# Performance work log

Hardware: AMD Instinct MI355X
Metric: run time of the kernel (lower is better)

The kernel has to match this reference:

```python
import jax, jax.numpy as jnp
import numpy as np

HEADS = 6
POINTS = 4
INJ_SHAPES = ((96, 96), (48, 48), (24, 24))  # adapter pyramid (H_l, W_l), sum = 12096 tokens
EXT_SHAPES = ((48, 48),)                      # vit grid level


def layernorm(x, g, b, eps=1e-6):
    m = jnp.mean(x, axis=-1, keepdims=True)
    v = jnp.mean((x - m) ** 2, axis=-1, keepdims=True)
    return (x - m) * jax.lax.rsqrt(v + eps) * g + b


def bilinear_sample(img, loc):
    # img: [B, heads, H, W, D]; loc: [B, heads, P, 2] normalized (x, y) in [0, 1]
    # matches F.grid_sample(mode='bilinear', padding_mode='zeros', align_corners=False)
    B, nh, H, W, D = img.shape
    flat = img.reshape(B, nh, H * W, D)
    ix = loc[..., 0] * W - 0.5
    iy = loc[..., 1] * H - 0.5
    x0f = jnp.floor(ix)
    y0f = jnp.floor(iy)
    wx = (ix - x0f)[..., None]
    wy = (iy - y0f)[..., None]
    x0 = x0f.astype(jnp.int32)
    y0 = y0f.astype(jnp.int32)

    def gather(xi, yi):
        valid = (xi >= 0) & (xi < W) & (yi >= 0) & (yi < H)
        idx = jnp.clip(yi, 0, H - 1) * W + jnp.clip(xi, 0, W - 1)
        g = jnp.take_along_axis(flat, idx[..., None], axis=2)
        return g * valid[..., None]

    v00 = gather(x0, y0)
    v01 = gather(x0 + 1, y0)
    v10 = gather(x0, y0 + 1)
    v11 = gather(x0 + 1, y0 + 1)
    return (v00 * (1 - wx) + v01 * wx) * (1 - wy) + (v10 * (1 - wx) + v11 * wx) * wy


def msda(query, value, ref, shapes, Wv, bv, Ws, bs_, Wa, ba, Wo, bo):
    # mmcv MultiScaleDeformableAttention (batch_first) without dropout/identity.
    B, Lq, C = query.shape
    D = C // HEADS
    L = len(shapes)
    v = (value @ Wv + bv).reshape(B, -1, HEADS, D)
    off = (query @ Ws + bs_).reshape(B, Lq, HEADS, L, POINTS, 2)
    aw = jax.nn.softmax((query @ Wa + ba).reshape(B, Lq, HEADS, L * POINTS), axis=-1)
    aw = aw.reshape(B, Lq, HEADS, L, POINTS)
    norm = jnp.array([[w, h] for (h, w) in shapes], dtype=query.dtype)  # (x, y) normalizer
    # ref: [B, Lq, 1, 2] broadcasts over heads/levels/points
    loc = ref[:, :, None, :, None, :] + off / norm[None, None, None, :, None, :]
    starts = np.cumsum([0] + [h * w for h, w in shapes])
    out = jnp.zeros((B, HEADS, Lq, D), query.dtype)
    for l, (h, w) in enumerate(shapes):
        vl = v[:, starts[l]:starts[l + 1]].reshape(B, h, w, HEADS, D).transpose(0, 3, 1, 2, 4)
        ll = loc[:, :, :, l].transpose(0, 2, 1, 3, 4).reshape(B, HEADS, Lq * POINTS, 2)
        s = bilinear_sample(vl, ll).reshape(B, HEADS, Lq, POINTS, D)
        out = out + jnp.einsum('bhqp,bhqpd->bhqd', aw[:, :, :, l].transpose(0, 2, 1, 3), s)
    out = out.transpose(0, 2, 1, 3).reshape(B, Lq, C)
    return out @ Wo + bo


def setup_inputs() -> dict:
    key = jax.random.key(0)
    ks = jax.random.split(key, 24)
    B, Hh, Ww, C = 1, 48, 48, 768
    NA = 12096  # 4*HW + HW + HW/4
    f32 = jnp.float32
    lin = lambda k, i, o, s=0.02: jax.random.normal(k, (i, o), f32) * s
    p = {
        'vit_feats': jax.random.normal(ks[0], (B, Hh, Ww, C), f32),
        'adapter_feats': jax.random.normal(ks[1], (B, NA, C), f32),
        'ref1': jax.random.uniform(ks[2], (B, Hh * Ww, 1, 2), f32),
        'ref2': jax.random.uniform(ks[3], (B, NA, 1, 2), f32),
        'inj_qn_g': jnp.ones((C,), f32), 'inj_qn_b': jnp.zeros((C,), f32),
        'inj_Wv': lin(ks[4], C, C), 'inj_bv': jnp.zeros((C,), f32),
        'inj_Ws': lin(ks[5], C, HEADS * 3 * POINTS * 2, 0.01),
        'inj_bs': jax.random.normal(ks[6], (HEADS * 3 * POINTS * 2,), f32),
        'inj_Wa': lin(ks[7], C, HEADS * 3 * POINTS), 'inj_ba': jnp.zeros((HEADS * 3 * POINTS,), f32),
        'inj_Wo': lin(ks[8], C, C), 'inj_bo': jnp.zeros((C,), f32),
        'inj_gamma': jax.random.normal(ks[9], (C,), f32) * 0.1,
        'ext_vn_g': jnp.ones((C,), f32), 'ext_vn_b': jnp.zeros((C,), f32),
        'ext_qn_g': jnp.ones((C,), f32), 'ext_qn_b': jnp.zeros((C,), f32),
        'ext_Wv': lin(ks[10], C, C), 'ext_bv': jnp.zeros((C,), f32),
        'ext_Ws': lin(ks[11], C, HEADS * 1 * POINTS * 2, 0.01),
        'ext_bs': jax.random.normal(ks[12], (HEADS * 1 * POINTS * 2,), f32),
        'ext_Wa': lin(ks[13], C, HEADS * 1 * POINTS), 'ext_ba': jnp.zeros((HEADS * 1 * POINTS,), f32),
        'ext_Wo': lin(ks[14], C, C), 'ext_bo': jnp.zeros((C,), f32),
        'H': 48, 'W': 48,
    }
    return p


def reference(vit_feats, adapter_feats, ref1, ref2,
              inj_qn_g, inj_qn_b, inj_Wv, inj_bv, inj_Ws, inj_bs, inj_Wa, inj_ba, inj_Wo, inj_bo, inj_gamma,
              ext_vn_g, ext_vn_b, ext_qn_g, ext_qn_b, ext_Wv, ext_bv, ext_Ws, ext_bs, ext_Wa, ext_ba, ext_Wo, ext_bo,
              H, W):
    b, h, w, c = vit_feats.shape
    q = vit_feats.reshape(b, h * w, c)
    # Injector: query = vit tokens, value = 3-level adapter pyramid; identity = 0, gamma-scaled residual
    attn = msda(layernorm(q, inj_qn_g, inj_qn_b), adapter_feats, ref1, INJ_SHAPES,
                inj_Wv, inj_bv, inj_Ws, inj_bs, inj_Wa, inj_ba, inj_Wo, inj_bo)
    q = q + inj_gamma * attn
    vit_out = q.reshape(b, h, w, c)
    # Extractor (with_cffn=False, v_pre_norm=True): value = LN(vit tokens), identity = adapter query, post query-norm
    value = layernorm(q, ext_vn_g, ext_vn_b)
    attn2 = msda(adapter_feats, value, ref2, EXT_SHAPES,
                 ext_Wv, ext_bv, ext_Ws, ext_bs, ext_Wa, ext_ba, ext_Wo, ext_bo)
    adapter_out = layernorm(adapter_feats + attn2, ext_qn_g, ext_qn_b)
    return vit_out, adapter_out
```

## Files before the change

### kernel.cpp

```cpp
#include <hip/hip_runtime.h>


#define LQ_VIT 2304
#define NA_ADA 12096

typedef float f32x4 __attribute__((ext_vector_type(4)));
typedef short bf16x8 __attribute__((ext_vector_type(8)));

__device__ __forceinline__ unsigned short f2bf(float f) {
  unsigned u = __builtin_bit_cast(unsigned, f);
  u += 0x7FFFu + ((u >> 16) & 1u);
  return (unsigned short)(u >> 16);
}
__device__ __forceinline__ float bf2f(unsigned short u) {
  return __builtin_bit_cast(float, (unsigned)u << 16);
}
__device__ __forceinline__ f32x4 ld4bf(const unsigned short* p) {
  ushort4 t = *(const ushort4*)p;
  f32x4 r; r[0] = bf2f(t.x); r[1] = bf2f(t.y); r[2] = bf2f(t.z); r[3] = bf2f(t.w);
  return r;
}

__device__ __forceinline__ void gload_lds16(const void* g, void* l) {
  __builtin_amdgcn_global_load_lds(
      (__attribute__((address_space(1))) void*)(void*)g,
      (__attribute__((address_space(3))) void*)l, 16, 0, 0);
}

struct PrepPack {
  const float* W[8];
  unsigned short* WT[8];
  int N[8];
  int cum[9];
  const float* adapter; unsigned short* adbf; int n4;
  const float* vit; const float* qg; const float* qb; unsigned short* qln;
  const float* isv; const float* iav; const float* ibv;
  const float* esv; const float* eav;
  float* bci; float* bbig;
};

__global__ __launch_bounds__(256) void prep_kernel(PrepPack pp) {
  int b = blockIdx.x;
  int tid = threadIdx.x;
  if (b < 2568) {
    int kb = b / 107, col = b % 107;
    int z = 0;
#pragma unroll
    for (int i = 0; i < 8; i++) if (col >= pp.cum[i + 1]) z = i + 1;
    int nb = col - pp.cum[z];
    const float* __restrict__ W = pp.W[z];
    unsigned short* __restrict__ WT = pp.WT[z];
    int N = pp.N[z];
    int kb32 = kb * 32, nb32 = nb * 32;
    __shared__ float tile[32][33];
    int tx = tid & 31, ty = tid >> 5;
    for (int i = ty; i < 32; i += 8) {
      int n = nb32 + tx;
      tile[i][tx] = (n < N) ? W[(size_t)(kb32 + i) * N + n] : 0.f;
    }
    __syncthreads();
    for (int i = ty; i < 32; i += 8) {
      int n = nb32 + i, k = kb32 + tx;
      if (n < N) WT[(size_t)n * 768 + k] = f2bf(tile[tx][i]);
    }
  } else if (b < 4616) {
    for (int i = (b - 2568) * 256 + tid; i < pp.n4; i += 2048 * 256) {
      float4 v = ((const float4*)pp.adapter)[i];
      ushort4 o;
      o.x = f2bf(v.x); o.y = f2bf(v.y); o.z = f2bf(v.z); o.w = f2bf(v.w);
      ((ushort4*)pp.adbf)[i] = o;
    }
  } else if (b < 5192) {
    int wid = (b - 4616) * 4 + (tid >> 6);
    int lane = tid & 63;
    if (wid >= LQ_VIT) return;
    const float* row = pp.vit + (size_t)wid * 768;
    float x[12]; float s = 0.f;
#pragma unroll
    for (int j = 0; j < 12; j++) { x[j] = row[lane + j * 64]; s += x[j]; }
#pragma unroll
    for (int o = 32; o >= 1; o >>= 1) s += __shfl_xor(s, o);
    float mean = s * (1.f / 768.f);
    float v = 0.f;
#pragma unroll
    for (int j = 0; j < 12; j++) { float d = x[j] - mean; v += d * d; }
#pragma unroll
    for (int o = 32; o >= 1; o >>= 1) v += __shfl_xor(v, o);
    float rs = rsqrtf(v * (1.f / 768.f) + 1e-6f);
#pragma unroll
    for (int j = 0; j < 12; j++) {
      int c = lane + j * 64;
      pp.qln[(size_t)wid * 768 + c] = f2bf((x[j] - mean) * rs * pp.qg[c] + pp.qb[c]);
    }
  } else {
    for (int i = tid; i < 840; i += 256) {
      if (i < 144) pp.bci[i] = pp.isv[i];
      else if (i < 216) pp.bci[i] = pp.iav[i - 144];
      if (i < 768) pp.bbig[i] = pp.ibv[i];
      else if (i < 816) pp.bbig[i] = pp.esv[i - 768];
      else pp.bbig[i] = pp.eav[i - 816];
    }
  }
}

struct GemmTask {
  const unsigned short* A; const unsigned short* BT;
  const float* bias; unsigned short* C;
  int M, N, NT, nwg;
};

__global__ __launch_bounds__(256, 2) void gemm_big_kernel(GemmTask t0, GemmTask t1, int split) {
  __shared__ unsigned short lds[2][(128 + 128) * 64];

  GemmTask tk = (blockIdx.x < split) ? t0 : t1;
  int id = (blockIdx.x < split) ? blockIdx.x : blockIdx.x - split;
  int nwg = tk.nwg;
  int qq = nwg >> 3, rr = nwg & 7;
  int xcd = id & 7, idx = id >> 3;
  int wg = (xcd < rr ? xcd * (qq + 1) : rr * (qq + 1) + (xcd - rr) * qq) + idx;
  int nt = wg % tk.NT, mt = wg / tk.NT;
  int m0 = mt * 128, n0 = nt * 128;
  int M = tk.M, N = tk.N;
  const unsigned short* __restrict__ A = tk.A;
  const unsigned short* __restrict__ BT = tk.BT;
  const int K = 768, kT = 12;

  int tid = threadIdx.x;
  int w = tid >> 6, lane = tid & 63;
  int wr = w >> 1, wc = w & 1;
  int frow = lane & 15, ghi = lane >> 4;
  int l7 = lane & 7;
  int sr = lane >> 3;
  int sgx = ((l7 ^ sr) * 8);
  int gx0 = ((ghi ^ l7) * 8);
  int gx1 = (((4 + ghi) ^ l7) * 8);

  f32x4 acc[4][4] = {};

  auto stage = [&](unsigned short* dst, int k0) {
#pragma unroll
    for (int i = 0; i < 8; i++) {
      int c = w * 8 + i;
      if (c < 16) {
        int gm = m0 + c * 8 + sr; if (gm >= M) gm = M - 1;
        gload_lds16(&A[(size_t)gm * K + k0 + sgx], &dst[c * 512]);
      } else {
        int gn = n0 + (c - 16) * 8 + sr; if (gn >= N) gn = N - 1;
        gload_lds16(&BT[(size_t)gn * K + k0 + sgx], &dst[c * 512]);
      }
    }
  };

  unsigned short* b0 = &lds[0][0];
  unsigned short* b1 = &lds[1][0];
  stage(b0, 0);
  __syncthreads();

  for (int t = 0; t < kT; t++) {
    unsigned short* cb = (t & 1) ? b1 : b0;
    unsigned short* nb = (t & 1) ? b0 : b1;
    if (t + 1 < kT) stage(nb, (t + 1) << 6);
    const unsigned short* As_ = cb;
    const unsigned short* Bs_ = cb + 16 * 512;
    bf16x8 af0[4], af1[4], bg0[4], bg1[4];
#pragma unroll
    for (int m = 0; m < 4; m++) {
      int r = wr * 64 + m * 16 + frow;
      af0[m] = *(const bf16x8*)&As_[r * 64 + gx0];
      af1[m] = *(const bf16x8*)&As_[r * 64 + gx1];
    }
#pragma unroll
    for (int n = 0; n < 4; n++) {
      int r = wc * 64 + n * 16 + frow;
      bg0[n] = *(const bf16x8*)&Bs_[r * 64 + gx0];
      bg1[n] = *(const bf16x8*)&Bs_[r * 64 + gx1];
    }
#pragma unroll
    for (int m = 0; m < 4; m++)
#pragma unroll
      for (int n = 0; n < 4; n++) {
        acc[m][n] = __builtin_amdgcn_mfma_f32_16x16x32_bf16(af0[m], bg0[n], acc[m][n], 0, 0, 0);
        acc[m][n] = __builtin_amdgcn_mfma_f32_16x16x32_bf16(af1[m], bg1[n], acc[m][n], 0, 0, 0);
      }
    __syncthreads();
  }

  int orow = (lane >> 4) * 4, ocol = lane & 15;
  unsigned short* C = tk.C;
  const float* bias = tk.bias;
#pragma unroll
  for (int m = 0; m < 4; m++) {
    int gmb = m0 + wr * 64 + m * 16 + orow;
#pragma unroll
    for (int n = 0; n < 4; n++) {
      int gn = n0 + wc * 64 + n * 16 + ocol;
      if (gn < N) {
        float bv = bias[gn];
#pragma unroll
        for (int r = 0; r < 4; r++) {
          int gm = gmb + r;
          if (gm < M) C[(size_t)gm * N + gn] = f2bf(acc[m][n][r] + bv);
        }
      }
    }
  }
}

__global__ __launch_bounds__(256) void gemm_mid_kernel(
    const unsigned short* __restrict__ A, const unsigned short* __restrict__ BT,
    const float* __restrict__ bias, unsigned short* __restrict__ C,
    int M, int N, int NT) {
  __shared__ unsigned short lds[2][(64 + 128) * 64];

  int nwg = gridDim.x;
  int id = blockIdx.x;
  int qq = nwg >> 3, rr = nwg & 7;
  int xcd = id & 7, idx = id >> 3;
  int wg = (xcd < rr ? xcd * (qq + 1) : rr * (qq + 1) + (xcd - rr) * qq) + idx;
  int nt = wg % NT, mt = wg / NT;
  int m0 = mt * 64, n0 = nt * 128;
  const int K = 768, kT = 12;

  int tid = threadIdx.x;
  int w = tid >> 6, lane = tid & 63;
  int frow = lane & 15, ghi = lane >> 4;
  int l7 = lane & 7;
  int sr = lane >> 3;
  int sgx = ((l7 ^ sr) * 8);
  int gx0 = ((ghi ^ l7) * 8);
  int gx1 = (((4 + ghi) ^ l7) * 8);

  f32x4 acc[4][2] = {};

  auto stage = [&](unsigned short* dst, int k0) {
#pragma unroll
    for (int i = 0; i < 6; i++) {
      int c = w * 6 + i;
      if (c < 8) {
        int gm = m0 + c * 8 + sr; if (gm >= M) gm = M - 1;
        gload_lds16(&A[(size_t)gm * K + k0 + sgx], &dst[c * 512]);
      } else {
        int gn = n0 + (c - 8) * 8 + sr; if (gn >= N) gn = N - 1;
        gload_lds16(&BT[(size_t)gn * K + k0 + sgx], &dst[c * 512]);
      }
    }
  };

  unsigned short* b0 = &lds[0][0];
  unsigned short* b1 = &lds[1][0];
  stage(b0, 0);
  __syncthreads();

  for (int t = 0; t < kT; t++) {
    unsigned short* cb = (t & 1) ? b1 : b0;
    unsigned short* nb = (t & 1) ? b0 : b1;
    if (t + 1 < kT) stage(nb, (t + 1) << 6);
    const unsigned short* As_ = cb;
    const unsigned short* Bs_ = cb + 8 * 512;
    bf16x8 af0[4], af1[4], bg0[2], bg1[2];
#pragma unroll
    for (int m = 0; m < 4; m++) {
      int r = m * 16 + frow;
      af0[m] = *(const bf16x8*)&As_[r * 64 + gx0];
      af1[m] = *(const bf16x8*)&As_[r * 64 + gx1];
    }
#pragma unroll
    for (int n = 0; n < 2; n++) {
      int r = w * 32 + n * 16 + frow;
      bg0[n] = *(const bf16x8*)&Bs_[r * 64 + gx0];
      bg1[n] = *(const bf16x8*)&Bs_[r * 64 + gx1];
    }
#pragma unroll
    for (int m = 0; m < 4; m++)
#pragma unroll
      for (int n = 0; n < 2; n++) {
        acc[m][n] = __builtin_amdgcn_mfma_f32_16x16x32_bf16(af0[m], bg0[n], acc[m][n], 0, 0, 0);
        acc[m][n] = __builtin_amdgcn_mfma_f32_16x16x32_bf16(af1[m], bg1[n], acc[m][n], 0, 0, 0);
      }
    __syncthreads();
  }

  int orow = (lane >> 4) * 4, ocol = lane & 15;
#pragma unroll
  for (int m = 0; m < 4; m++) {
    int gmb = m0 + m * 16 + orow;
#pragma unroll
    for (int n = 0; n < 2; n++) {
      int gn = n0 + w * 32 + n * 16 + ocol;
      if (gn < N) {
        float bv = bias[gn];
#pragma unroll
        for (int r = 0; r < 4; r++) {
          int gm = gmb + r;
          if (gm < M) C[(size_t)gm * N + gn] = f2bf(acc[m][n][r] + bv);
        }
      }
    }
  }
}

__global__ __launch_bounds__(256) void residual_ln_kernel(
    const float* __restrict__ vit, const unsigned short* __restrict__ attn,
    const float* __restrict__ gamma, const float* __restrict__ g,
    const float* __restrict__ b, float* __restrict__ vout,
    unsigned short* __restrict__ vln, int R) {
  int wid = blockIdx.x * 4 + (threadIdx.x >> 6);
  int lane = threadIdx.x & 63;
  if (wid >= R) return;
  const float* ra = vit + (size_t)wid * 768;
  const unsigned short* rb = attn + (size_t)wid * 768;
  float x[12]; float s = 0.f;
#pragma unroll
  for (int j = 0; j < 12; j++) {
    int c = lane + j * 64;
    x[j] = ra[c] + gamma[c] * bf2f(rb[c]);
    vout[(size_t)wid * 768 + c] = x[j];
    s += x[j];
  }
#pragma unroll
  for (int o = 32; o >= 1; o >>= 1) s += __shfl_xor(s, o);
  float mean = s * (1.f / 768.f);
  float v = 0.f;
#pragma unroll
  for (int j = 0; j < 12; j++) { float d = x[j] - mean; v += d * d; }
#pragma unroll
  for (int o = 32; o >= 1; o >>= 1) v += __shfl_xor(v, o);
  float rs = rsqrtf(v * (1.f / 768.f) + 1e-6f);
#pragma unroll
  for (int j = 0; j < 12; j++) {
    int c = lane + j * 64;
    vln[(size_t)wid * 768 + c] = f2bf((x[j] - mean) * rs * g[c] + b[c]);
  }
}

__global__ __launch_bounds__(256) void add_ln_f32_kernel(
    const float* __restrict__ Xa, const unsigned short* __restrict__ Xb,
    const float* __restrict__ g, const float* __restrict__ b,
    float* __restrict__ out, int R) {
  int wid = blockIdx.x * 4 + (threadIdx.x >> 6);
  int lane = threadIdx.x & 63;
  if (wid >= R) return;
  const float* ra = Xa + (size_t)wid * 768;
  const unsigned short* rb = Xb + (size_t)wid * 768;
  float x[12]; float s = 0.f;
#pragma unroll
  for (int j = 0; j < 12; j++) {
    int c = lane + j * 64;
    x[j] = ra[c] + bf2f(rb[c]); s += x[j];
  }
#pragma unroll
  for (int o = 32; o >= 1; o >>= 1) s += __shfl_xor(s, o);
  float mean = s * (1.f / 768.f);
  float v = 0.f;
#pragma unroll
  for (int j = 0; j < 12; j++) { float d = x[j] - mean; v += d * d; }
#pragma unroll
  for (int o = 32; o >= 1; o >>= 1) v += __shfl_xor(v, o);
  float rs = rsqrtf(v * (1.f / 768.f) + 1e-6f);
#pragma unroll
  for (int j = 0; j < 12; j++) {
    int c = lane + j * 64;
    out[(size_t)wid * 768 + c] = (x[j] - mean) * rs * g[c] + b[c];
  }
}

__global__ __launch_bounds__(256) void sampler_inj_kernel(
    const float* __restrict__ ref, const unsigned short* __restrict__ sa,
    const unsigned short* __restrict__ v, unsigned short* __restrict__ out, int vst) {
  int gw = (blockIdx.x * 256 + threadIdx.x) >> 6;
  int lane = threadIdx.x & 63;
  int q = gw / 3, hp = gw - q * 3;
  if (q >= LQ_VIT) return;
  int h = hp * 2 + (lane >> 5);
  int c = h * 128 + (lane & 31) * 4;
  float rx = ref[q * 2], ry = ref[q * 2 + 1];
  const unsigned short* row = sa + (size_t)q * 216;
  float lg[12]; float mx = -1e30f;
#pragma unroll
  for (int i = 0; i < 12; i++) { lg[i] = bf2f(row[144 + h * 12 + i]); mx = fmaxf(mx, lg[i]); }
  float s = 0.f;
#pragma unroll
  for (int i = 0; i < 12; i++) { lg[i] = __expf(lg[i] - mx); s += lg[i]; }
  float inv = 1.f / s;
  f32x4 acc = {0.f, 0.f, 0.f, 0.f};
  const int LW[3] = {96, 48, 24};
  const int LS[3] = {0, 9216, 11520};
#pragma unroll
  for (int l = 0; l < 3; l++) {
    const int Wl = LW[l], st = LS[l], Wm = Wl - 1;
    const float Wf = (float)Wl;
#pragma unroll
    for (int p = 0; p < 4; p++) {
      int ob = ((h * 3 + l) * 4 + p) * 2;
      float ix = fmaf(rx, Wf, bf2f(row[ob])) - 0.5f;
      float iy = fmaf(ry, Wf, bf2f(row[ob + 1])) - 0.5f;
      float x0f = floorf(ix), y0f = floorf(iy);
      float wx = ix - x0f, wy = iy - y0f;
      int x0 = (int)x0f, y0 = (int)y0f;
      float aw = lg[l * 4 + p] * inv;
      float wy0 = (1.f - wy) * aw, wy1 = wy * aw;
      float w00 = (1.f - wx) * wy0, w01 = wx * wy0;
      float w10 = (1.f - wx) * wy1, w11 = wx * wy1;
      bool xv0 = (unsigned)x0 < (unsigned)Wl, xv1 = (unsigned)(x0 + 1) < (unsigned)Wl;
      bool yv0 = (unsigned)y0 < (unsigned)Wl, yv1 = (unsigned)(y0 + 1) < (unsigned)Wl;
      w00 = (xv0 && yv0) ? w00 : 0.f;
      w01 = (xv1 && yv0) ? w01 : 0.f;
      w10 = (xv0 && yv1) ? w10 : 0.f;
      w11 = (xv1 && yv1) ? w11 : 0.f;
      int x0c = min(max(x0, 0), Wm), x1c = min(max(x0 + 1, 0), Wm);
      int y0c = min(max(y0, 0), Wm), y1c = min(max(y0 + 1, 0), Wm);
      const unsigned short* r0 = v + ((size_t)(st + y0c * Wl) * vst + c);
      const unsigned short* r1 = v + ((size_t)(st + y1c * Wl) * vst + c);
      acc += w00 * ld4bf(r0 + (size_t)x0c * vst) + w01 * ld4bf(r0 + (size_t)x1c * vst)
           + w10 * ld4bf(r1 + (size_t)x0c * vst) + w11 * ld4bf(r1 + (size_t)x1c * vst);
    }
  }
  ushort4 o4;
  o4.x = f2bf(acc[0]); o4.y = f2bf(acc[1]); o4.z = f2bf(acc[2]); o4.w = f2bf(acc[3]);
  *(ushort4*)&out[(size_t)q * 768 + c] = o4;
}

__global__ __launch_bounds__(256) void sampler_ext_kernel(
    const float* __restrict__ ref, const unsigned short* __restrict__ sa, int sst,
    const unsigned short* __restrict__ v, unsigned short* __restrict__ out) {
  int gw = (blockIdx.x * 256 + threadIdx.x) >> 6;
  int lane = threadIdx.x & 63;
  int q = gw / 3, hp = gw - q * 3;
  if (q >= NA_ADA) return;
  int h = hp * 2 + (lane >> 5);
  int c = h * 128 + (lane & 31) * 4;
  float rx = ref[q * 2], ry = ref[q * 2 + 1];
  const unsigned short* row = sa + (size_t)q * sst;
  float lg[4]; float mx = -1e30f;
#pragma unroll
  for (int p = 0; p < 4; p++) { lg[p] = bf2f(row[48 + h * 4 + p]); mx = fmaxf(mx, lg[p]); }
  float s = 0.f;
#pragma unroll
  for (int p = 0; p < 4; p++) { lg[p] = __expf(lg[p] - mx); s += lg[p]; }
  float inv = 1.f / s;
  f32x4 acc = {0.f, 0.f, 0.f, 0.f};
#pragma unroll
  for (int p = 0; p < 4; p++) {
    int ob = (h * 4 + p) * 2;
    float ix = fmaf(rx, 48.f, bf2f(row[ob])) - 0.5f;
    float iy = fmaf(ry, 48.f, bf2f(row[ob + 1])) - 0.5f;
    float x0f = floorf(ix), y0f = floorf(iy);
    float wx = ix - x0f, wy = iy - y0f;
    int x0 = (int)x0f, y0 = (int)y0f;
    float aw = lg[p] * inv;
    float wy0 = (1.f - wy) * aw, wy1 = wy * aw;
    float w00 = (1.f - wx) * wy0, w01 = wx * wy0;
    float w10 = (1.f - wx) * wy1, w11 = wx * wy1;
    bool xv0 = (unsigned)x0 < 48u, xv1 = (unsigned)(x0 + 1) < 48u;
    bool yv0 = (unsigned)y0 < 48u, yv1 = (unsigned)(y0 + 1) < 48u;
    w00 = (xv0 && yv0) ? w00 : 0.f;
    w01 = (xv1 && yv0) ? w01 : 0.f;
    w10 = (xv0 && yv1) ? w10 : 0.f;
    w11 = (xv1 && yv1) ? w11 : 0.f;
    int x0c = min(max(x0, 0), 47), x1c = min(max(x0 + 1, 0), 47);
    int y0c = min(max(y0, 0), 47), y1c = min(max(y0 + 1, 0), 47);
    const unsigned short* r0 = v + ((size_t)(y0c * 48) * 768 + c);
    const unsigned short* r1 = v + ((size_t)(y1c * 48) * 768 + c);
    acc += w00 * ld4bf(r0 + (size_t)x0c * 768) + w01 * ld4bf(r0 + (size_t)x1c * 768)
         + w10 * ld4bf(r1 + (size_t)x0c * 768) + w11 * ld4bf(r1 + (size_t)x1c * 768);
  }
  ushort4 o4;
  o4.x = f2bf(acc[0]); o4.y = f2bf(acc[1]); o4.z = f2bf(acc[2]); o4.w = f2bf(acc[3]);
  *(ushort4*)&out[(size_t)q * 768 + c] = o4;
}

extern "C" void kernel_launch(void* const* d_in, const int* in_sizes, int n_in,
                              void* d_out, int out_size, void* d_ws, size_t ws_size,
                              hipStream_t stream) {
  (void)in_sizes; (void)n_in; (void)out_size; (void)ws_size;
  const float* vit      = (const float*)d_in[0];
  const float* adapter  = (const float*)d_in[1];
  const float* ref1     = (const float*)d_in[2];
  const float* ref2     = (const float*)d_in[3];
  const float* inj_qn_g = (const float*)d_in[4];
  const float* inj_qn_b = (const float*)d_in[5];
  const float* inj_Wv   = (const float*)d_in[6];
  const float* inj_bv   = (const float*)d_in[7];
  const float* inj_Ws   = (const float*)d_in[8];
  const float* inj_bs   = (const float*)d_in[9];
  const float* inj_Wa   = (const float*)d_in[10];
  const float* inj_ba   = (const float*)d_in[11];
  const float* inj_Wo   = (const float*)d_in[12];
  const float* inj_bo   = (const float*)d_in[13];
  const float* inj_gamma= (const float*)d_in[14];
  const float* ext_vn_g = (const float*)d_in[15];
  const float* ext_vn_b = (const float*)d_in[16];
  const float* ext_qn_g = (const float*)d_in[17];
  const float* ext_qn_b = (const float*)d_in[18];
  const float* ext_Wv   = (const float*)d_in[19];
  const float* ext_bv   = (const float*)d_in[20];
  const float* ext_Ws   = (const float*)d_in[21];
  const float* ext_bs   = (const float*)d_in[22];
  const float* ext_Wa   = (const float*)d_in[23];
  const float* ext_ba   = (const float*)d_in[24];
  const float* ext_Wo   = (const float*)d_in[25];
  const float* ext_bo   = (const float*)d_in[26];

  size_t cur = 0;
  auto take = [&](size_t bytes) {
    void* p = (char*)d_ws + cur;
    cur += (bytes + 255) & ~(size_t)255;
    return p;
  };
  unsigned short* WBIG = (unsigned short*)take((size_t)840 * 768 * 2);
  unsigned short* WTIO = (unsigned short*)take((size_t)768 * 768 * 2);
  unsigned short* WTEV = (unsigned short*)take((size_t)768 * 768 * 2);
  unsigned short* WTEO = (unsigned short*)take((size_t)768 * 768 * 2);
  unsigned short* WSAI = (unsigned short*)take((size_t)216 * 768 * 2);
  float* BCI  = (float*)take((size_t)216 * 4);
  float* BBIG = (float*)take((size_t)840 * 4);
  unsigned short* ADBF = (unsigned short*)take((size_t)NA_ADA * 768 * 2);
  unsigned short* QLN  = (unsigned short*)take((size_t)LQ_VIT * 768 * 2);
  unsigned short* CBIG = (unsigned short*)take((size_t)NA_ADA * 840 * 2);
  unsigned short* SAI  = (unsigned short*)take((size_t)LQ_VIT * 216 * 2);
  unsigned short* SAMPI= (unsigned short*)take((size_t)LQ_VIT * 768 * 2);
  unsigned short* ATTNI= (unsigned short*)take((size_t)LQ_VIT * 768 * 2);
  unsigned short* VLN  = (unsigned short*)take((size_t)LQ_VIT * 768 * 2);
  unsigned short* VEXT = (unsigned short*)take((size_t)LQ_VIT * 768 * 2);
  unsigned short* SAMPE = ADBF;
  unsigned short* ATTN2 = CBIG;

  float* out_vit = (float*)d_out;
  float* out_ada = out_vit + (size_t)LQ_VIT * 768;

  PrepPack pp;
  pp.W[0] = inj_Wv; pp.WT[0] = WBIG;               pp.N[0] = 768;
  pp.W[1] = ext_Ws; pp.WT[1] = WBIG + 768 * 768;   pp.N[1] = 48;
  pp.W[2] = ext_Wa; pp.WT[2] = WBIG + 816 * 768;   pp.N[2] = 24;
  pp.W[3] = inj_Wo; pp.WT[3] = WTIO;               pp.N[3] = 768;
  pp.W[4] = ext_Wv; pp.WT[4] = WTEV;               pp.N[4] = 768;
  pp.W[5] = ext_Wo; pp.WT[5] = WTEO;               pp.N[5] = 768;
  pp.W[6] = inj_Ws; pp.WT[6] = WSAI;               pp.N[6] = 144;
  pp.W[7] = inj_Wa; pp.WT[7] = WSAI + 144 * 768;   pp.N[7] = 72;
  int cum = 0;
  for (int i = 0; i < 8; i++) { pp.cum[i] = cum; cum += (pp.N[i] + 31) / 32; }
  pp.cum[8] = cum;
  pp.adapter = adapter; pp.adbf = ADBF; pp.n4 = (NA_ADA * 768) / 4;
  pp.vit = vit; pp.qg = inj_qn_g; pp.qb = inj_qn_b; pp.qln = QLN;
  pp.isv = inj_bs; pp.iav = inj_ba; pp.ibv = inj_bv;
  pp.esv = ext_bs; pp.eav = ext_ba;
  pp.bci = BCI; pp.bbig = BBIG;
  prep_kernel<<<5193, 256, 0, stream>>>(pp);

  GemmTask tA, tB;
  tA.A = ADBF; tA.BT = WBIG; tA.bias = BBIG; tA.C = CBIG;
  tA.M = NA_ADA; tA.N = 840; tA.NT = 7; tA.nwg = 95 * 7;
  tB.A = QLN; tB.BT = WSAI; tB.bias = BCI; tB.C = SAI;
  tB.M = LQ_VIT; tB.N = 216; tB.NT = 2; tB.nwg = 18 * 2;
  gemm_big_kernel<<<95 * 7 + 18 * 2, 256, 0, stream>>>(tA, tB, 95 * 7);

  sampler_inj_kernel<<<1728, 256, 0, stream>>>(ref1, SAI, CBIG, SAMPI, 840);

  gemm_mid_kernel<<<36 * 6, 256, 0, stream>>>(SAMPI, WTIO, inj_bo, ATTNI, LQ_VIT, 768, 6);
  residual_ln_kernel<<<576, 256, 0, stream>>>(vit, ATTNI, inj_gamma, ext_vn_g, ext_vn_b,
                                              out_vit, VLN, LQ_VIT);
  gemm_mid_kernel<<<36 * 6, 256, 0, stream>>>(VLN, WTEV, ext_bv, VEXT, LQ_VIT, 768, 6);

  sampler_ext_kernel<<<9072, 256, 0, stream>>>(ref2, CBIG + 768, 840, VEXT, SAMPE);

  GemmTask tC;
  tC.A = SAMPE; tC.BT = WTEO; tC.bias = ext_bo; tC.C = ATTN2;
  tC.M = NA_ADA; tC.N = 768; tC.NT = 6; tC.nwg = 95 * 6;
  gemm_big_kernel<<<95 * 6, 256, 0, stream>>>(tC, tC, 95 * 6);

  add_ln_f32_kernel<<<3024, 256, 0, stream>>>(adapter, ATTN2, ext_qn_g, ext_qn_b, out_ada, NA_ADA);
}
```

Measured before the change: 186.7 us.

## Replace double-buffered LDS staging in big GEMM with single buffer

```diff
diff --git a/kernel.cpp b/kernel.cpp
--- a/kernel.cpp
+++ b/kernel.cpp
@@ -109,8 +109,8 @@
   int M, N, NT, nwg;
 };
 
-__global__ __launch_bounds__(256, 2) void gemm_big_kernel(GemmTask t0, GemmTask t1, int split) {
-  __shared__ unsigned short lds[2][(128 + 128) * 64];
+__global__ __launch_bounds__(256) void gemm_big_kernel(GemmTask t0, GemmTask t1, int split) {
+  __shared__ unsigned short lds[(128 + 128) * 64];
 
   GemmTask tk = (blockIdx.x < split) ? t0 : t1;
   int id = (blockIdx.x < split) ? blockIdx.x : blockIdx.x - split;
@@ -137,52 +137,54 @@
 
   f32x4 acc[4][4] = {};
 
-  auto stage = [&](unsigned short* dst, int k0) {
+  auto stage = [&](int k0) {
 #pragma unroll
     for (int i = 0; i < 8; i++) {
       int c = w * 8 + i;
       if (c < 16) {
         int gm = m0 + c * 8 + sr; if (gm >= M) gm = M - 1;
-        gload_lds16(&A[(size_t)gm * K + k0 + sgx], &dst[c * 512]);
+        gload_lds16(&A[(size_t)gm * K + k0 + sgx], &lds[c * 512]);
       } else {
         int gn = n0 + (c - 16) * 8 + sr; if (gn >= N) gn = N - 1;
-        gload_lds16(&BT[(size_t)gn * K + k0 + sgx], &dst[c * 512]);
+        gload_lds16(&BT[(size_t)gn * K + k0 + sgx], &lds[c * 512]);
       }
     }
   };
 
-  unsigned short* b0 = &lds[0][0];
-  unsigned short* b1 = &lds[1][0];
-  stage(b0, 0);
-  __syncthreads();
-
   for (int t = 0; t < kT; t++) {
-    unsigned short* cb = (t & 1) ? b1 : b0;
-    unsigned short* nb = (t & 1) ? b0 : b1;
-    if (t + 1 < kT) stage(nb, (t + 1) << 6);
-    const unsigned short* As_ = cb;
-    const unsigned short* Bs_ = cb + 16 * 512;
-    bf16x8 af0[4], af1[4], bg0[4], bg1[4];
-#pragma unroll
-    for (int m = 0; m < 4; m++) {
-      int r = wr * 64 + m * 16 + frow;
-      af0[m] = *(const bf16x8*)&As_[r * 64 + gx0];
-      af1[m] = *(const bf16x8*)&As_[r * 64 + gx1];
-    }
-#pragma unroll
-    for (int n = 0; n < 4; n++) {
-      int r = wc * 64 + n * 16 + frow;
-      bg0[n] = *(const bf16x8*)&Bs_[r * 64 + gx0];
-      bg1[n] = *(const bf16x8*)&Bs_[r * 64 + gx1];
-    }
-#pragma unroll
-    for (int m = 0; m < 4; m++)
-#pragma unroll
-      for (int n = 0; n < 4; n++) {
-        acc[m][n] = __builtin_amdgcn_mfma_f32_16x16x32_bf16(af0[m], bg0[n], acc[m][n], 0, 0, 0);
-        acc[m][n] = __builtin_amdgcn_mfma_f32_16x16x32_bf16(af1[m], bg1[n], acc[m][n], 0, 0, 0);
-      }
     __syncthreads();
+    stage(t << 6);
+    __syncthreads();
+    const unsigned short* As_ = lds;
+    const unsigned short* Bs_ = lds + 16 * 512;
+    {
+      bf16x8 af[4], bg[4];
+#pragma unroll
+      for (int m = 0; m < 4; m++)
+        af[m] = *(const bf16x8*)&As_[(wr * 64 + m * 16 + frow) * 64 + gx0];
+#pragma unroll
+      for (int n = 0; n < 4; n++)
+        bg[n] = *(const bf16x8*)&Bs_[(wc * 64 + n * 16 + frow) * 64 + gx0];
+#pragma unroll
+      for (int m = 0; m < 4; m++)
+#pragma unroll
+        for (int n = 0; n < 4; n++)
+          acc[m][n] = __builtin_amdgcn_mfma_f32_16x16x32_bf16(af[m], bg[n], acc[m][n], 0, 0, 0);
+    }
+    {
+      bf16x8 af[4], bg[4];
+#pragma unroll
+      for (int m = 0; m < 4; m++)
+        af[m] = *(const bf16x8*)&As_[(wr * 64 + m * 16 + frow) * 64 + gx1];
+#pragma unroll
+      for (int n = 0; n < 4; n++)
+        bg[n] = *(const bf16x8*)&Bs_[(wc * 64 + n * 16 + frow) * 64 + gx1];
+#pragma unroll
+      for (int m = 0; m < 4; m++)
+#pragma unroll
+        for (int n = 0; n < 4; n++)
+          acc[m][n] = __builtin_amdgcn_mfma_f32_16x16x32_bf16(af[m], bg[n], acc[m][n], 0, 0, 0);
+    }
   }
 
   int orow = (lane >> 4) * 4, ocol = lane & 15;
```

New measurement: 200.8 us. 1.08x slower.
